# Kernel optimization log

Measured on AMD Instinct MI355X. Metric: run time of the kernel, lower is better.

Reference implementation:

```python
import jax, jax.numpy as jnp
import numpy as np

NUM_SKILLS = 50000
HIDDEN = 64
B, T = 8192, 1024
EPS = 1e-6


def setup_inputs() -> dict:
    key = jax.random.key(0)
    ks = jax.random.split(key, 8)
    X = jax.random.randint(ks[0], (B,), 0, NUM_SKILLS)
    y = jax.random.randint(ks[1], (B, T), 0, 2, dtype=jnp.int32)
    embed = jax.random.normal(ks[2], (NUM_SKILLS, HIDDEN), jnp.float32)
    bound = 1.0 / np.sqrt(HIDDEN)
    W0 = jax.random.uniform(ks[3], (HIDDEN, HIDDEN), jnp.float32, -bound, bound)
    b0 = jnp.zeros((HIDDEN,), jnp.float32)
    W1 = jax.random.uniform(ks[4], (HIDDEN, HIDDEN), jnp.float32, -bound, bound)
    b1 = jnp.zeros((HIDDEN,), jnp.float32)
    Wout = jax.random.uniform(ks[5], (HIDDEN, 4), jnp.float32, -bound, bound)
    bout = jnp.zeros((4,), jnp.float32)
    return {"X": X, "y": y, "embed": embed, "W0": W0, "b0": b0,
            "W1": W1, "b1": b1, "Wout": Wout, "bout": bout}


def reference(X, y, embed, W0, b0, W1, b1, Wout, bout):
    # Per-student BKT params from embedding + 2-layer MLP + sigmoid, clamped
    h = embed[X]                                   # (B, H)
    h = jax.nn.relu(h @ W0 + b0)
    h = jax.nn.relu(h @ W1 + b1)
    params = jnp.clip(jax.nn.sigmoid(h @ Wout + bout), EPS, 1.0 - EPS)  # (B, 4)
    l, g, s, prior = params[:, 0], params[:, 1], params[:, 2], params[:, 3]

    def step(latent, y_t):
        true_correct = jnp.where(y_t == -1, 0, y_t)
        correct = latent * (1.0 - s) + (1.0 - latent) * g
        k_t1 = latent * (1.0 - s) / correct
        k_t0 = latent * s / (latent * s + (1.0 - latent) * (1.0 - g))
        k_t = jnp.where(true_correct > 0.5, k_t1, k_t0)
        next_latent = jnp.clip(k_t + (1.0 - k_t) * l, EPS, 1.0 - EPS)
        return next_latent, (correct, latent)

    _, (corrects, latents) = jax.lax.scan(step, prior, y.T)  # scan over T
    return corrects.T, latents.T                            # (B, T) each
```

## Files before the change

### kernel.cpp

```cpp
#include <hip/hip_runtime.h>

#define TSTEPS 1024
#define NROWS  8192
#define CLEN   16
#define KEPS   1e-6f

__device__ __forceinline__ float clampP(float x) {
    return fminf(fmaxf(x, KEPS), 1.f - KEPS);
}
__device__ __forceinline__ float sigm(float v) {
    return 1.0f / (1.0f + __expf(-v));
}

__global__ __launch_bounds__(256) void bkt_params_v4(
    const int* __restrict__ X, const float* __restrict__ embed,
    const float* __restrict__ W0, const float* __restrict__ b0,
    const float* __restrict__ W1, const float* __restrict__ b1,
    const float* __restrict__ Wout, const float* __restrict__ bout,
    float4* __restrict__ params)
{
    const int lane    = threadIdx.x & 63;
    const int wid     = threadIdx.x >> 6;
    const int rowbase = blockIdx.x * 16 + wid * 4;

    __shared__ float sh[4][4][64];
    float (*shw)[64] = sh[wid];

    #pragma unroll
    for (int rs = 0; rs < 4; ++rs) {
        const int skill = X[rowbase + rs];
        shw[rs][lane] = embed[(size_t)skill * 64 + lane];
    }
    __syncthreads();

    float a0 = b0[lane], a1 = a0, a2 = a0, a3 = a0;
    #pragma unroll
    for (int k4 = 0; k4 < 16; ++k4) {
        const float4 e0 = *(const float4*)&shw[0][k4 * 4];
        const float4 e1 = *(const float4*)&shw[1][k4 * 4];
        const float4 e2 = *(const float4*)&shw[2][k4 * 4];
        const float4 e3 = *(const float4*)&shw[3][k4 * 4];
        const float w0 = W0[(k4 * 4 + 0) * 64 + lane];
        const float w1 = W0[(k4 * 4 + 1) * 64 + lane];
        const float w2 = W0[(k4 * 4 + 2) * 64 + lane];
        const float w3 = W0[(k4 * 4 + 3) * 64 + lane];
        a0 = fmaf(e0.x, w0, a0); a0 = fmaf(e0.y, w1, a0); a0 = fmaf(e0.z, w2, a0); a0 = fmaf(e0.w, w3, a0);
        a1 = fmaf(e1.x, w0, a1); a1 = fmaf(e1.y, w1, a1); a1 = fmaf(e1.z, w2, a1); a1 = fmaf(e1.w, w3, a1);
        a2 = fmaf(e2.x, w0, a2); a2 = fmaf(e2.y, w1, a2); a2 = fmaf(e2.z, w2, a2); a2 = fmaf(e2.w, w3, a2);
        a3 = fmaf(e3.x, w0, a3); a3 = fmaf(e3.y, w1, a3); a3 = fmaf(e3.z, w2, a3); a3 = fmaf(e3.w, w3, a3);
    }
    __syncthreads();
    shw[0][lane] = fmaxf(a0, 0.f);
    shw[1][lane] = fmaxf(a1, 0.f);
    shw[2][lane] = fmaxf(a2, 0.f);
    shw[3][lane] = fmaxf(a3, 0.f);
    __syncthreads();

    a0 = b1[lane]; a1 = a0; a2 = a0; a3 = a0;
    #pragma unroll
    for (int k4 = 0; k4 < 16; ++k4) {
        const float4 e0 = *(const float4*)&shw[0][k4 * 4];
        const float4 e1 = *(const float4*)&shw[1][k4 * 4];
        const float4 e2 = *(const float4*)&shw[2][k4 * 4];
        const float4 e3 = *(const float4*)&shw[3][k4 * 4];
        const float w0 = W1[(k4 * 4 + 0) * 64 + lane];
        const float w1 = W1[(k4 * 4 + 1) * 64 + lane];
        const float w2 = W1[(k4 * 4 + 2) * 64 + lane];
        const float w3 = W1[(k4 * 4 + 3) * 64 + lane];
        a0 = fmaf(e0.x, w0, a0); a0 = fmaf(e0.y, w1, a0); a0 = fmaf(e0.z, w2, a0); a0 = fmaf(e0.w, w3, a0);
        a1 = fmaf(e1.x, w0, a1); a1 = fmaf(e1.y, w1, a1); a1 = fmaf(e1.z, w2, a1); a1 = fmaf(e1.w, w3, a1);
        a2 = fmaf(e2.x, w0, a2); a2 = fmaf(e2.y, w1, a2); a2 = fmaf(e2.z, w2, a2); a2 = fmaf(e2.w, w3, a2);
        a3 = fmaf(e3.x, w0, a3); a3 = fmaf(e3.y, w1, a3); a3 = fmaf(e3.z, w2, a3); a3 = fmaf(e3.w, w3, a3);
    }
    const float h0r = fmaxf(a0, 0.f), h1r = fmaxf(a1, 0.f);
    const float h2r = fmaxf(a2, 0.f), h3r = fmaxf(a3, 0.f);

    const float4 wo = ((const float4*)Wout)[lane];
    float p[4][4];
    p[0][0] = h0r * wo.x; p[0][1] = h0r * wo.y; p[0][2] = h0r * wo.z; p[0][3] = h0r * wo.w;
    p[1][0] = h1r * wo.x; p[1][1] = h1r * wo.y; p[1][2] = h1r * wo.z; p[1][3] = h1r * wo.w;
    p[2][0] = h2r * wo.x; p[2][1] = h2r * wo.y; p[2][2] = h2r * wo.z; p[2][3] = h2r * wo.w;
    p[3][0] = h3r * wo.x; p[3][1] = h3r * wo.y; p[3][2] = h3r * wo.z; p[3][3] = h3r * wo.w;
    #pragma unroll
    for (int off = 32; off >= 1; off >>= 1) {
        #pragma unroll
        for (int rs = 0; rs < 4; ++rs)
            #pragma unroll
            for (int c = 0; c < 4; ++c)
                p[rs][c] += __shfl_xor(p[rs][c], off, 64);
    }
    const float4 bo = *(const float4*)bout;
    float v0 = (lane == 0) ? p[0][0] : (lane == 1) ? p[1][0] : (lane == 2) ? p[2][0] : p[3][0];
    float v1 = (lane == 0) ? p[0][1] : (lane == 1) ? p[1][1] : (lane == 2) ? p[2][1] : p[3][1];
    float v2 = (lane == 0) ? p[0][2] : (lane == 1) ? p[1][2] : (lane == 2) ? p[2][2] : p[3][2];
    float v3 = (lane == 0) ? p[0][3] : (lane == 1) ? p[1][3] : (lane == 2) ? p[2][3] : p[3][3];
    if (lane < 4) {
        float4 r;
        r.x = clampP(sigm(v0 + bo.x));
        r.y = clampP(sigm(v1 + bo.y));
        r.z = clampP(sigm(v2 + bo.z));
        r.w = clampP(sigm(v3 + bo.w));
        params[rowbase + lane] = r;
    }
}

__global__ __launch_bounds__(256) void bkt_scan_v4(
    const int* __restrict__ y, const float4* __restrict__ params,
    float* __restrict__ out_corr, float* __restrict__ out_lat)
{
    const int lane = threadIdx.x & 63;
    const int row  = blockIdx.x * 4 + (threadIdx.x >> 6);

    const float4 p = params[row];
    const float l = p.x, g = p.y, s = p.z, prior = p.w;

    const int4* yb = (const int4*)(y + (size_t)row * TSTEPS + lane * CLEN);
    const int4 v0 = yb[0], v1 = yb[1], v2 = yb[2], v3 = yb[3];
    unsigned msk = 0;
    msk |= (v0.x > 0) ? 1u << 0  : 0u; msk |= (v0.y > 0) ? 1u << 1  : 0u;
    msk |= (v0.z > 0) ? 1u << 2  : 0u; msk |= (v0.w > 0) ? 1u << 3  : 0u;
    msk |= (v1.x > 0) ? 1u << 4  : 0u; msk |= (v1.y > 0) ? 1u << 5  : 0u;
    msk |= (v1.z > 0) ? 1u << 6  : 0u; msk |= (v1.w > 0) ? 1u << 7  : 0u;
    msk |= (v2.x > 0) ? 1u << 8  : 0u; msk |= (v2.y > 0) ? 1u << 9  : 0u;
    msk |= (v2.z > 0) ? 1u << 10 : 0u; msk |= (v2.w > 0) ? 1u << 11 : 0u;
    msk |= (v3.x > 0) ? 1u << 12 : 0u; msk |= (v3.y > 0) ? 1u << 13 : 0u;
    msk |= (v3.z > 0) ? 1u << 14 : 0u; msk |= (v3.w > 0) ? 1u << 15 : 0u;

    const float c1 = 1.f - s - g, d1 = g;
    const float e00_1 = fmaf(l, c1, (1.f - l) * (1.f - s));
    const float e01_1 = l * d1;
    const float c0 = s + g - 1.f, d0 = 1.f - g;
    const float e00_0 = fmaf(l, c0, (1.f - l) * s);
    const float e01_0 = l * d0;

    float m00 = 1.f, m01 = 0.f, m10 = 0.f, m11 = 1.f;
    #pragma unroll
    for (int t = 0; t < CLEN; ++t) {
        const bool one = (msk >> t) & 1u;
        const float e00 = one ? e00_1 : e00_0;
        const float e01 = one ? e01_1 : e01_0;
        const float e10 = one ? c1 : c0;
        const float e11 = one ? d1 : d0;
        const float n00 = fmaf(e00, m00, e01 * m10);
        const float n01 = fmaf(e00, m01, e01 * m11);
        const float n10 = fmaf(e10, m00, e11 * m10);
        const float n11 = fmaf(e10, m01, e11 * m11);
        if ((t & 3) == 3) {
            const float inv = __builtin_amdgcn_rcpf(n11);
            m00 = n00 * inv; m01 = n01 * inv; m10 = n10 * inv; m11 = 1.f;
        } else {
            m00 = n00; m01 = n01; m10 = n10; m11 = n11;
        }
    }

    float s00 = m00, s01 = m01, s10 = m10, s11 = m11;
    #pragma unroll
    for (int d = 1; d < 64; d <<= 1) {
        const float t00 = __shfl_up(s00, d, 64);
        const float t01 = __shfl_up(s01, d, 64);
        const float t10 = __shfl_up(s10, d, 64);
        const float t11 = __shfl_up(s11, d, 64);
        if (lane >= d) {
            const float r00 = fmaf(s00, t00, s01 * t10);
            const float r01 = fmaf(s00, t01, s01 * t11);
            const float r10 = fmaf(s10, t00, s11 * t10);
            const float r11 = fmaf(s10, t01, s11 * t11);
            const float inv = __builtin_amdgcn_rcpf(r11);
            s00 = r00 * inv; s01 = r01 * inv; s10 = r10 * inv; s11 = 1.f;
        }
    }
    const float x00 = __shfl_up(s00, 1, 64);
    const float x01 = __shfl_up(s01, 1, 64);
    const float x10 = __shfl_up(s10, 1, 64);
    const float x11 = __shfl_up(s11, 1, 64);
    float L0;
    if (lane == 0) {
        L0 = prior;
    } else {
        const float num = fmaf(x00, prior, x01);
        const float den = fmaf(x10, prior, x11);
        L0 = clampP(num * __builtin_amdgcn_rcpf(den));
    }

    const float a   = 1.f - s;
    const float omg = 1.f - g;
    const float oml = 1.f - l;
    float* oc = out_corr + (size_t)row * TSTEPS + lane * CLEN;
    float* ol = out_lat  + (size_t)row * TSTEPS + lane * CLEN;
    float Lc = L0;
    #pragma unroll
    for (int w = 0; w < 4; ++w) {
        float cr[4], lt[4];
        #pragma unroll
        for (int q = 0; q < 4; ++q) {
            const int t = w * 4 + q;
            const float correct = fmaf(Lc, c1, g);
            const float den0    = fmaf(Lc, c0, omg);
            const float k1 = (Lc * a) * __builtin_amdgcn_rcpf(correct);
            const float k0 = (Lc * s) * __builtin_amdgcn_rcpf(den0);
            const bool one = (msk >> t) & 1u;
            const float k = one ? k1 : k0;
            cr[q] = correct;
            lt[q] = Lc;
            Lc = clampP(fmaf(k, oml, l));
        }
        *(float4*)(oc + w * 4) = make_float4(cr[0], cr[1], cr[2], cr[3]);
        *(float4*)(ol + w * 4) = make_float4(lt[0], lt[1], lt[2], lt[3]);
    }
}

extern "C" void kernel_launch(void* const* d_in, const int* in_sizes, int n_in,
                              void* d_out, int out_size, void* d_ws, size_t ws_size,
                              hipStream_t stream) {
    const int*   X     = (const int*)  d_in[0];
    const int*   y     = (const int*)  d_in[1];
    const float* embed = (const float*)d_in[2];
    const float* W0    = (const float*)d_in[3];
    const float* b0    = (const float*)d_in[4];
    const float* W1    = (const float*)d_in[5];
    const float* b1    = (const float*)d_in[6];
    const float* Wout  = (const float*)d_in[7];
    const float* bout  = (const float*)d_in[8];

    float* out_corr = (float*)d_out;
    float* out_lat  = out_corr + (size_t)NROWS * TSTEPS;
    float4* paramsb = (float4*)d_ws;

    bkt_params_v4<<<NROWS / 16, 256, 0, stream>>>(X, embed, W0, b0, W1, b1, Wout, bout, paramsb);
    bkt_scan_v4 <<<NROWS / 4,  256, 0, stream>>>(y, paramsb, out_corr, out_lat);
}
```

Before: 132.6 us.

## Fuse per-row parameter MLP into scan kernel, one wave per row

Replaces the separate parameter kernel and the workspace round trip with a single kernel. Each wavefront now computes its own row's embedding-MLP-sigmoid parameters while the y loads are in flight, then runs the scan. This removes one kernel launch and the global write and read of the params buffer. In exchange, the MLP weights are loaded redundantly by every wave rather than shared across four rows. It also relies on intra-wave LDS ordering with no barrier between the shared-memory write and the subsequent reads.

```diff
diff --git a/kernel.cpp b/kernel.cpp
--- a/kernel.cpp
+++ b/kernel.cpp
@@ -12,107 +12,19 @@
     return 1.0f / (1.0f + __expf(-v));
 }
 
-__global__ __launch_bounds__(256) void bkt_params_v4(
-    const int* __restrict__ X, const float* __restrict__ embed,
+__global__ __launch_bounds__(256) void bkt_onewave(
+    const int* __restrict__ X, const int* __restrict__ y,
+    const float* __restrict__ embed,
     const float* __restrict__ W0, const float* __restrict__ b0,
     const float* __restrict__ W1, const float* __restrict__ b1,
     const float* __restrict__ Wout, const float* __restrict__ bout,
-    float4* __restrict__ params)
-{
-    const int lane    = threadIdx.x & 63;
-    const int wid     = threadIdx.x >> 6;
-    const int rowbase = blockIdx.x * 16 + wid * 4;
-
-    __shared__ float sh[4][4][64];
-    float (*shw)[64] = sh[wid];
-
-    #pragma unroll
-    for (int rs = 0; rs < 4; ++rs) {
-        const int skill = X[rowbase + rs];
-        shw[rs][lane] = embed[(size_t)skill * 64 + lane];
-    }
-    __syncthreads();
-
-    float a0 = b0[lane], a1 = a0, a2 = a0, a3 = a0;
-    #pragma unroll
-    for (int k4 = 0; k4 < 16; ++k4) {
-        const float4 e0 = *(const float4*)&shw[0][k4 * 4];
-        const float4 e1 = *(const float4*)&shw[1][k4 * 4];
-        const float4 e2 = *(const float4*)&shw[2][k4 * 4];
-        const float4 e3 = *(const float4*)&shw[3][k4 * 4];
-        const float w0 = W0[(k4 * 4 + 0) * 64 + lane];
-        const float w1 = W0[(k4 * 4 + 1) * 64 + lane];
-        const float w2 = W0[(k4 * 4 + 2) * 64 + lane];
-        const float w3 = W0[(k4 * 4 + 3) * 64 + lane];
-        a0 = fmaf(e0.x, w0, a0); a0 = fmaf(e0.y, w1, a0); a0 = fmaf(e0.z, w2, a0); a0 = fmaf(e0.w, w3, a0);
-        a1 = fmaf(e1.x, w0, a1); a1 = fmaf(e1.y, w1, a1); a1 = fmaf(e1.z, w2, a1); a1 = fmaf(e1.w, w3, a1);
-        a2 = fmaf(e2.x, w0, a2); a2 = fmaf(e2.y, w1, a2); a2 = fmaf(e2.z, w2, a2); a2 = fmaf(e2.w, w3, a2);
-        a3 = fmaf(e3.x, w0, a3); a3 = fmaf(e3.y, w1, a3); a3 = fmaf(e3.z, w2, a3); a3 = fmaf(e3.w, w3, a3);
-    }
-    __syncthreads();
-    shw[0][lane] = fmaxf(a0, 0.f);
-    shw[1][lane] = fmaxf(a1, 0.f);
-    shw[2][lane] = fmaxf(a2, 0.f);
-    shw[3][lane] = fmaxf(a3, 0.f);
-    __syncthreads();
-
-    a0 = b1[lane]; a1 = a0; a2 = a0; a3 = a0;
-    #pragma unroll
-    for (int k4 = 0; k4 < 16; ++k4) {
-        const float4 e0 = *(const float4*)&shw[0][k4 * 4];
-        const float4 e1 = *(const float4*)&shw[1][k4 * 4];
-        const float4 e2 = *(const float4*)&shw[2][k4 * 4];
-        const float4 e3 = *(const float4*)&shw[3][k4 * 4];
-        const float w0 = W1[(k4 * 4 + 0) * 64 + lane];
-        const float w1 = W1[(k4 * 4 + 1) * 64 + lane];
-        const float w2 = W1[(k4 * 4 + 2) * 64 + lane];
-        const float w3 = W1[(k4 * 4 + 3) * 64 + lane];
-        a0 = fmaf(e0.x, w0, a0); a0 = fmaf(e0.y, w1, a0); a0 = fmaf(e0.z, w2, a0); a0 = fmaf(e0.w, w3, a0);
-        a1 = fmaf(e1.x, w0, a1); a1 = fmaf(e1.y, w1, a1); a1 = fmaf(e1.z, w2, a1); a1 = fmaf(e1.w, w3, a1);
-        a2 = fmaf(e2.x, w0, a2); a2 = fmaf(e2.y, w1, a2); a2 = fmaf(e2.z, w2, a2); a2 = fmaf(e2.w, w3, a2);
-        a3 = fmaf(e3.x, w0, a3); a3 = fmaf(e3.y, w1, a3); a3 = fmaf(e3.z, w2, a3); a3 = fmaf(e3.w, w3, a3);
-    }
-    const float h0r = fmaxf(a0, 0.f), h1r = fmaxf(a1, 0.f);
-    const float h2r = fmaxf(a2, 0.f), h3r = fmaxf(a3, 0.f);
-
-    const float4 wo = ((const float4*)Wout)[lane];
-    float p[4][4];
-    p[0][0] = h0r * wo.x; p[0][1] = h0r * wo.y; p[0][2] = h0r * wo.z; p[0][3] = h0r * wo.w;
-    p[1][0] = h1r * wo.x; p[1][1] = h1r * wo.y; p[1][2] = h1r * wo.z; p[1][3] = h1r * wo.w;
-    p[2][0] = h2r * wo.x; p[2][1] = h2r * wo.y; p[2][2] = h2r * wo.z; p[2][3] = h2r * wo.w;
-    p[3][0] = h3r * wo.x; p[3][1] = h3r * wo.y; p[3][2] = h3r * wo.z; p[3][3] = h3r * wo.w;
-    #pragma unroll
-    for (int off = 32; off >= 1; off >>= 1) {
-        #pragma unroll
-        for (int rs = 0; rs < 4; ++rs)
-            #pragma unroll
-            for (int c = 0; c < 4; ++c)
-                p[rs][c] += __shfl_xor(p[rs][c], off, 64);
-    }
-    const float4 bo = *(const float4*)bout;
-    float v0 = (lane == 0) ? p[0][0] : (lane == 1) ? p[1][0] : (lane == 2) ? p[2][0] : p[3][0];
-    float v1 = (lane == 0) ? p[0][1] : (lane == 1) ? p[1][1] : (lane == 2) ? p[2][1] : p[3][1];
-    float v2 = (lane == 0) ? p[0][2] : (lane == 1) ? p[1][2] : (lane == 2) ? p[2][2] : p[3][2];
-    float v3 = (lane == 0) ? p[0][3] : (lane == 1) ? p[1][3] : (lane == 2) ? p[2][3] : p[3][3];
-    if (lane < 4) {
-        float4 r;
-        r.x = clampP(sigm(v0 + bo.x));
-        r.y = clampP(sigm(v1 + bo.y));
-        r.z = clampP(sigm(v2 + bo.z));
-        r.w = clampP(sigm(v3 + bo.w));
-        params[rowbase + lane] = r;
-    }
-}
-
-__global__ __launch_bounds__(256) void bkt_scan_v4(
-    const int* __restrict__ y, const float4* __restrict__ params,
     float* __restrict__ out_corr, float* __restrict__ out_lat)
 {
     const int lane = threadIdx.x & 63;
-    const int row  = blockIdx.x * 4 + (threadIdx.x >> 6);
+    const int wid  = threadIdx.x >> 6;
+    const int row  = blockIdx.x * 4 + wid;
 
-    const float4 p = params[row];
-    const float l = p.x, g = p.y, s = p.z, prior = p.w;
+    __shared__ float sh[4][64];
 
     const int4* yb = (const int4*)(y + (size_t)row * TSTEPS + lane * CLEN);
     const int4 v0 = yb[0], v1 = yb[1], v2 = yb[2], v3 = yb[3];
@@ -125,6 +37,46 @@
     msk |= (v2.z > 0) ? 1u << 10 : 0u; msk |= (v2.w > 0) ? 1u << 11 : 0u;
     msk |= (v3.x > 0) ? 1u << 12 : 0u; msk |= (v3.y > 0) ? 1u << 13 : 0u;
     msk |= (v3.z > 0) ? 1u << 14 : 0u; msk |= (v3.w > 0) ? 1u << 15 : 0u;
+
+    const int skill = X[row];
+    sh[wid][lane] = embed[(size_t)skill * 64 + lane];
+
+    float acc = b0[lane];
+    #pragma unroll
+    for (int k4 = 0; k4 < 16; ++k4) {
+        const float4 e = *(const float4*)&sh[wid][k4 * 4];
+        acc = fmaf(e.x, W0[(k4 * 4 + 0) * 64 + lane], acc);
+        acc = fmaf(e.y, W0[(k4 * 4 + 1) * 64 + lane], acc);
+        acc = fmaf(e.z, W0[(k4 * 4 + 2) * 64 + lane], acc);
+        acc = fmaf(e.w, W0[(k4 * 4 + 3) * 64 + lane], acc);
+    }
+    sh[wid][lane] = fmaxf(acc, 0.f);
+
+    acc = b1[lane];
+    #pragma unroll
+    for (int k4 = 0; k4 < 16; ++k4) {
+        const float4 e = *(const float4*)&sh[wid][k4 * 4];
+        acc = fmaf(e.x, W1[(k4 * 4 + 0) * 64 + lane], acc);
+        acc = fmaf(e.y, W1[(k4 * 4 + 1) * 64 + lane], acc);
+        acc = fmaf(e.z, W1[(k4 * 4 + 2) * 64 + lane], acc);
+        acc = fmaf(e.w, W1[(k4 * 4 + 3) * 64 + lane], acc);
+    }
+    const float h1v = fmaxf(acc, 0.f);
+
+    const float4 wo = ((const float4*)Wout)[lane];
+    float p0 = h1v * wo.x, p1 = h1v * wo.y, p2 = h1v * wo.z, p3 = h1v * wo.w;
+    #pragma unroll
+    for (int off = 32; off >= 1; off >>= 1) {
+        p0 += __shfl_xor(p0, off, 64);
+        p1 += __shfl_xor(p1, off, 64);
+        p2 += __shfl_xor(p2, off, 64);
+        p3 += __shfl_xor(p3, off, 64);
+    }
+    const float4 bo = *(const float4*)bout;
+    const float l     = clampP(sigm(p0 + bo.x));
+    const float g     = clampP(sigm(p1 + bo.y));
+    const float s     = clampP(sigm(p2 + bo.z));
+    const float prior = clampP(sigm(p3 + bo.w));
 
     const float c1 = 1.f - s - g, d1 = g;
     const float e00_1 = fmaf(l, c1, (1.f - l) * (1.f - s));
@@ -224,8 +176,7 @@
 
     float* out_corr = (float*)d_out;
     float* out_lat  = out_corr + (size_t)NROWS * TSTEPS;
-    float4* paramsb = (float4*)d_ws;
 
-    bkt_params_v4<<<NROWS / 16, 256, 0, stream>>>(X, embed, W0, b0, W1, b1, Wout, bout, paramsb);
-    bkt_scan_v4 <<<NROWS / 4,  256, 0, stream>>>(y, paramsb, out_corr, out_lat);
+    bkt_onewave<<<NROWS / 4, 256, 0, stream>>>(X, y, embed, W0, b0, W1, b1, Wout, bout,
+                                               out_corr, out_lat);
 }
```

Result: no change. 132.9 us (+0.2%).
